# Optimization experiments

Measured on AMD Instinct MI355X. Metric: run time of the kernel, lower is better.

Reference implementation:

```python
import math
import jax, jax.numpy as jnp
from jax import lax
import numpy as np

B, S, D = 64, 257, 768
H, HD = 12, 64  # heads, head_dim; D == H*HD


def setup_inputs() -> dict:
    key = jax.random.key(0)
    ks = jax.random.split(key, 12)
    sc = 0.02
    return {
        "hidden_states": jax.random.normal(ks[0], (B, S, D), jnp.float32),
        "Wq": jax.random.normal(ks[1], (D, D), jnp.float32) * sc,
        "bq": jax.random.normal(ks[2], (D,), jnp.float32) * sc,
        "Wk": jax.random.normal(ks[3], (D, D), jnp.float32) * sc,
        "bk": jax.random.normal(ks[4], (D,), jnp.float32) * sc,
        "Wv": jax.random.normal(ks[5], (D, D), jnp.float32) * sc,
        "bv": jax.random.normal(ks[6], (D,), jnp.float32) * sc,
        "Wo": jax.random.normal(ks[7], (D, D), jnp.float32) * sc,
        "bo": jax.random.normal(ks[8], (D,), jnp.float32) * sc,
        "conv1_w": jax.random.normal(ks[9], (D, 1, 1, 1), jnp.float32) * sc,
        "conv2_w": jax.random.normal(ks[10], (D, 1, 3, 3), jnp.float32) * sc,
        "conv3_w": jax.random.normal(ks[11], (D, 1, 5, 5), jnp.float32) * sc,
    }


def reference(hidden_states, Wq, bq, Wk, bk, Wv, bv, Wo, bo, conv1_w, conv2_w, conv3_w):
    scale = 1.0 / math.sqrt(HD)
    # Q over full sequence (cls + 256 patches)
    q = (hidden_states @ Wq.T + bq).reshape(B, S, H, HD).transpose(0, 2, 1, 3)  # [B,H,S,HD]
    cls_tok = hidden_states[:, :1]                                   # [B,1,D]
    x = hidden_states[:, 1:].transpose(0, 2, 1).reshape(B, D, 16, 16)  # NCHW
    ctx = jnp.zeros((B, H, S, HD), hidden_states.dtype)
    for cw in (conv1_w, conv2_w, conv3_w):  # depthwise convs, VALID padding
        xb = lax.conv_general_dilated(x, cw, (1, 1), 'VALID',
                                      feature_group_count=D)         # [B,D,h,w]
        xb = xb.reshape(B, D, -1).transpose(0, 2, 1)                  # [B,L-1,D]
        xb = jnp.concatenate([cls_tok, xb], axis=1)                   # [B,L,D]
        L = xb.shape[1]
        k = (xb @ Wk.T + bk).reshape(B, L, H, HD).transpose(0, 2, 1, 3)
        v = (xb @ Wv.T + bv).reshape(B, L, H, HD).transpose(0, 2, 1, 3)
        scores = jnp.einsum('bhqd,bhkd->bhqk', q, k) * scale
        probs = jax.nn.softmax(scores, axis=-1)
        ctx = ctx + jnp.einsum('bhqk,bhkd->bhqd', probs, v)
    ctx = (ctx / 3.0).transpose(0, 2, 1, 3).reshape(B, S, D)
    return ctx @ Wo.T + bo
```

## Files before the change

### kernel.cpp

```cpp
#include <hip/hip_runtime.h>

using bf16   = __bf16;
using bf16x4 = __bf16 __attribute__((ext_vector_type(4)));
using bf16x8 = __bf16 __attribute__((ext_vector_type(8)));
using f32x4  = float __attribute__((ext_vector_type(4)));

#define MFMA_BF16(a, b, c) __builtin_amdgcn_mfma_f32_16x16x32_bf16((a), (b), (c), 0, 0, 0)

constexpr int BATCH = 64, SEQ = 257, DIM = 768, NH = 12;
constexpr size_t WE = (size_t)DIM * DIM;

__device__ inline void gload_lds16(const bf16* g, bf16* l) {
  __builtin_amdgcn_global_load_lds(
      (const __attribute__((address_space(1))) void*)g,
      (__attribute__((address_space(3))) void*)l, 16, 0, 0);
}

__global__ __launch_bounds__(256) void cvt_weights(
    const float* __restrict__ wq, const float* __restrict__ wk,
    const float* __restrict__ wv, const float* __restrict__ wo,
    bf16* __restrict__ dst) {
  const size_t i = (size_t)blockIdx.x * 256 + threadIdx.x;
  const size_t per = WE / 4;
  if (i >= 4 * per) return;
  const float* srcs[4] = {wq, wk, wv, wo};
  const float4 f = ((const float4*)srcs[i / per])[i % per];
  bf16* o = dst + i * 4;
  o[0] = (bf16)f.x; o[1] = (bf16)f.y; o[2] = (bf16)f.z; o[3] = (bf16)f.w;
}

__global__ __launch_bounds__(256) void cvt_hs(const float* __restrict__ src,
                                              bf16* __restrict__ dst, int n4) {
  const int i = blockIdx.x * 256 + threadIdx.x;
  if (i >= n4) return;
  const float4 f = ((const float4*)src)[i];
  bf16* o = dst + (size_t)i * 4;
  o[0] = (bf16)f.x; o[1] = (bf16)f.y; o[2] = (bf16)f.z; o[3] = (bf16)f.w;
}

template <int KS>
__global__ __launch_bounds__(256) void conv_kernel(
    const float* __restrict__ hs, const float* __restrict__ cw, bf16* __restrict__ xb) {
  constexpr int OW = 17 - KS;
  constexpr int NOUT = OW * OW;
  constexpr int L = NOUT + 1;
  constexpr int KSQ = KS * KS;
  constexpr int NP = (NOUT + 7) / 8;
  __shared__ float hsl[256][36];
  __shared__ float wsm[32][KSQ];

  const int t = threadIdx.x;
  const int b = blockIdx.y;
  const int c0 = blockIdx.x * 32;

  const float* src = hs + ((size_t)b * SEQ + 1 + t) * DIM + c0;
#pragma unroll
  for (int j = 0; j < 8; ++j) *(float4*)&hsl[t][4 * j] = ((const float4*)src)[j];

  if (t < 32) {
#pragma unroll
    for (int q = 0; q < KSQ; ++q) wsm[t][q] = cw[(size_t)(c0 + t) * KSQ + q];
    const float cv = hs[(size_t)b * SEQ * DIM + c0 + t];
    xb[(size_t)b * L * DIM + c0 + t] = (bf16)cv;
  }
  __syncthreads();

  const int c = t & 31, pg = t >> 5;
#pragma unroll
  for (int i = 0; i < NP; ++i) {
    const int p = pg * NP + i;
    if (p < NOUT) {
      const int oi = p / OW, oj = p - oi * OW;
      float a = 0.f;
#pragma unroll
      for (int di = 0; di < KS; ++di)
#pragma unroll
        for (int dj = 0; dj < KS; ++dj)
          a += hsl[(oi + di) * 16 + oj + dj][c] * wsm[c][di * KS + dj];
      xb[((size_t)b * L + 1 + p) * DIM + c0 + c] = (bf16)a;
    }
  }
}

template <int OUT>
__global__ __launch_bounds__(256, 4) void gemm_lds_kernel(
    const bf16* __restrict__ A, const bf16* __restrict__ W,
    const float* __restrict__ bias0, const float* __restrict__ bias1,
    void* __restrict__ Y0, void* __restrict__ Y1, int M, int L, int Lv, int nN) {
  constexpr int BUF_E = 128 * 32;
  __shared__ alignas(16) bf16 sm[6 * BUF_E];
  bf16* smA = sm;
  bf16* smB = sm + 3 * BUF_E;

  const int tid = threadIdx.x;
  const int lane = tid & 63;
  const int w = tid >> 6;

  const int nwg = gridDim.x;
  const int orig = blockIdx.x;
  const int nq = nwg >> 3, rr = nwg & 7, xcd = orig & 7, base = orig >> 3;
  const int wgid = (xcd < rr ? xcd * (nq + 1) : rr * (nq + 1) + (xcd - rr) * nq) + base;
  const int tM = wgid / nN, tN = wgid - tM * nN;

  const int wr = (w >> 1) * 64, wc = (w & 1) * 64;
  const int rl = lane & 15;
  const int g = lane >> 4;
  const int kqs = ((g ^ ((rl >> 1) & 3)) << 3);

  const int sr = lane >> 2;
  const int sk = (((lane & 3) ^ ((sr >> 1) & 3)) << 3);
  const int r0 = w * 32 + sr;
  const int r1 = w * 32 + 16 + sr;
  long ga0 = (long)tM * 128 + r0; if (ga0 >= M) ga0 = M - 1;
  long ga1 = (long)tM * 128 + r1; if (ga1 >= M) ga1 = M - 1;
  const bf16* pa0 = A + ga0 * DIM + sk;
  const bf16* pa1 = A + ga1 * DIM + sk;
  const bf16* pb0 = W + ((size_t)tN * 128 + r0) * DIM + sk;
  const bf16* pb1 = W + ((size_t)tN * 128 + r1) * DIM + sk;
  const int lbase = (w * 32) * 32;

  const f32x4 zero4 = {0.f, 0.f, 0.f, 0.f};
  f32x4 acc[4][4];
#pragma unroll
  for (int m = 0; m < 4; ++m)
#pragma unroll
    for (int n = 0; n < 4; ++n) acc[m][n] = zero4;

  constexpr int NT = DIM / 32;

#define STAGE(kt_, buf_)                                      \
  do {                                                        \
    const int kb_ = (kt_) * 32;                               \
    bf16* a_ = smA + (buf_) * BUF_E + lbase;                  \
    bf16* b_ = smB + (buf_) * BUF_E + lbase;                  \
    gload_lds16(pa0 + kb_, a_);                               \
    gload_lds16(pa1 + kb_, a_ + 512);                         \
    gload_lds16(pb0 + kb_, b_);                               \
    gload_lds16(pb1 + kb_, b_ + 512);                         \
  } while (0)

  STAGE(0, 0);
  STAGE(1, 1);
  asm volatile("s_waitcnt vmcnt(4)" ::: "memory");
  __builtin_amdgcn_s_barrier();
  __builtin_amdgcn_sched_barrier(0);

  int buf = 0;
  for (int kt = 0; kt < NT; ++kt) {
    const bf16* Ac = smA + buf * BUF_E;
    const bf16* Bc = smB + buf * BUF_E;
    bf16x8 af[4], bfr[4];
#pragma unroll
    for (int m = 0; m < 4; ++m) af[m] = *(const bf16x8*)&Ac[(wr + m * 16 + rl) * 32 + kqs];
#pragma unroll
    for (int n = 0; n < 4; ++n) bfr[n] = *(const bf16x8*)&Bc[(wc + n * 16 + rl) * 32 + kqs];
#pragma unroll
    for (int m = 0; m < 4; ++m)
#pragma unroll
      for (int n = 0; n < 4; ++n) acc[m][n] = MFMA_BF16(af[m], bfr[n], acc[m][n]);

    if (kt + 2 < NT) {
      const int nb = buf + 2 >= 3 ? buf - 1 : buf + 2;
      STAGE(kt + 2, nb);
    }
    if (kt + 1 < NT) {
      if (kt + 2 < NT) asm volatile("s_waitcnt vmcnt(4)" ::: "memory");
      else             asm volatile("s_waitcnt vmcnt(0)" ::: "memory");
      __builtin_amdgcn_s_barrier();
      __builtin_amdgcn_sched_barrier(0);
    }
    buf = buf == 2 ? 0 : buf + 1;
  }
#undef STAGE

  if constexpr (OUT == 3) {
#pragma unroll
    for (int n = 0; n < 4; ++n) {
      const int gcol = tN * 128 + wc + n * 16 + rl;
      const float bia = bias0[gcol];
#pragma unroll
      for (int m = 0; m < 4; ++m) {
#pragma unroll
        for (int i = 0; i < 4; ++i) {
          const long grow = (long)tM * 128 + wr + m * 16 + g * 4 + i;
          if (grow < M) ((float*)Y0)[grow * DIM + gcol] = acc[m][n][i] + bia;
        }
      }
    }
    return;
  }

  constexpr int TP = 136;
  bf16* smT = sm;
  __syncthreads();

  const bool vpath = (OUT == 1) && (tN >= 6);
  if (vpath) {
#pragma unroll
    for (int n = 0; n < 4; ++n) {
      const int col = wc + n * 16 + rl;
      const float bia = bias1[tN * 128 + col - 768];
#pragma unroll
      for (int m = 0; m < 4; ++m) {
        const int row = wr + m * 16 + g * 4;
        bf16x4 v4;
#pragma unroll
        for (int i = 0; i < 4; ++i) v4[i] = (bf16)(acc[m][n][i] + bia);
        *(bf16x4*)(smT + col * TP + row) = v4;
      }
    }
    __syncthreads();
    bf16* vout = (bf16*)Y1;
    const int tNv = tN - 6;
#pragma unroll
    for (int it = 0; it < 8; ++it) {
      const int c = it * 256 + tid;
      const int coll = c >> 4;
      const int rw0 = (c & 15) * 8;
      const long g2 = (long)tM * 128 + rw0;
      if (g2 < M) {
        const int b2 = (int)(g2 / L);
        const int l2 = (int)(g2 - (long)b2 * L);
        const int cv = tNv * 128 + coll;
        bf16* dst = vout + (((size_t)b2 * NH + (cv >> 6)) * 64 + (cv & 63)) * Lv;
        const bf16x8 v = *(const bf16x8*)(smT + coll * TP + rw0);
        if (l2 + 8 <= L) {
          *(bf16x8*)(dst + l2) = v;
        } else {
#pragma unroll
          for (int j = 0; j < 8; ++j) {
            const long g3 = g2 + j;
            const int b3 = (int)(g3 / L), l3 = (int)(g3 - (long)b3 * L);
            vout[(((size_t)b3 * NH + (cv >> 6)) * 64 + (cv & 63)) * Lv + l3] = v[j];
          }
        }
      }
    }
  } else {
    const float scale = (OUT == 0) ? 0.125f : 1.f;
#pragma unroll
    for (int n = 0; n < 4; ++n) {
      const int col = wc + n * 16 + rl;
      const float bia = bias0[tN * 128 + col];
#pragma unroll
      for (int m = 0; m < 4; ++m) {
#pragma unroll
        for (int i = 0; i < 4; ++i) {
          const int row = wr + m * 16 + g * 4 + i;
          smT[row * TP + col] = (bf16)((acc[m][n][i] + bia) * scale);
        }
      }
    }
    __syncthreads();
    bf16* kout = (bf16*)Y0;
#pragma unroll
    for (int it = 0; it < 8; ++it) {
      const int c = it * 256 + tid;
      const int row = c >> 4;
      const int col0 = (c & 15) * 8;
      const long g2 = (long)tM * 128 + row;
      if (g2 < M) {
        const int b2 = (int)(g2 / L);
        const int l2 = (int)(g2 - (long)b2 * L);
        const int gc = tN * 128 + col0;
        const bf16x8 v = *(const bf16x8*)(smT + row * TP + col0);
        int dchunk = (gc & 63) >> 3;
        if constexpr (OUT == 1) dchunk ^= (l2 & 7);
        *(bf16x8*)(kout + (((size_t)b2 * NH + (gc >> 6)) * L + l2) * 64 + dchunk * 8) = v;
      }
    }
  }
}

template <int L, int BRANCH>
__global__ __launch_bounds__(256, 2) void attn_kernel(
    const bf16* __restrict__ qb, const bf16* __restrict__ kb, const bf16* __restrict__ vb,
    float* __restrict__ ctx, bf16* __restrict__ xbuf, int Lv) {
  constexpr int LK16 = (L + 15) & ~15;
  constexpr int NKT = LK16 / 16;
  constexpr int LP32 = (L + 31) & ~31;
  constexpr int NK32 = LP32 / 32;
  constexpr int PSTR = LP32 + 8;
  __shared__ alignas(16) bf16 Ks[LK16 * 64];
  __shared__ alignas(16) bf16 Ps[64 * PSTR];

  const int tid = threadIdx.x, lane = tid & 63, w = tid >> 6;
  const int orig = blockIdx.x;
  const int nper = gridDim.x >> 3;
  const int bh = (orig & 7) * nper + (orig >> 3);
  const int b = bh / NH, h = bh % NH;
  const int cl = lane & 15, g = lane >> 4;

  const bf16* kbase = kb + (size_t)bh * L * 64;
  for (int c = tid; c < LK16 * 8; c += 256)
    gload_lds16(kbase + (size_t)c * 8, Ks + (size_t)c * 8);
  __syncthreads();

  const bf16* vbase = vb + (size_t)bh * 64 * Lv;

  for (int qt = 0; qt < 5; ++qt) {
    int sq = qt * 64 + w * 16 + cl;
    if (sq > 256) sq = 256;
    const bf16* qrow = qb + ((size_t)bh * 257 + sq) * 64 + g * 8;
    const bf16x8 aq0 = *(const bf16x8*)qrow;
    const bf16x8 aq1 = *(const bf16x8*)(qrow + 32);

    float sums[4] = {0.f, 0.f, 0.f, 0.f};
    const int prow0 = (w * 16 + g * 4) * PSTR + cl;
#pragma unroll
    for (int kt = 0; kt < NKT; ++kt) {
      const int key0 = kt * 16 + cl;
      const int sw = key0 & 7;
      const char* krow = (const char*)Ks + key0 * 128;
      const bf16x8 bk0 = *(const bf16x8*)(krow + ((g ^ sw) << 4));
      const bf16x8 bk1 = *(const bf16x8*)(krow + (((4 + g) ^ sw) << 4));
      f32x4 z = {0.f, 0.f, 0.f, 0.f};
      z = MFMA_BF16(aq0, bk0, z);
      z = MFMA_BF16(aq1, bk1, z);
      const bool valid = key0 < L;
#pragma unroll
      for (int j = 0; j < 4; ++j) {
        const float p = valid ? __expf(z[j]) : 0.f;
        sums[j] += p;
        Ps[prow0 + j * PSTR + kt * 16] = (bf16)p;
      }
    }
    if constexpr (LP32 > LK16) {
#pragma unroll
      for (int j = 0; j < 4; ++j) Ps[prow0 + j * PSTR + LK16] = (bf16)0.f;
    }

    bf16x8 vr0[4], vr1[4];
#pragma unroll
    for (int nt = 0; nt < 4; ++nt)
      vr0[nt] = *(const bf16x8*)(vbase + (size_t)(nt * 16 + cl) * Lv + g * 8);

#pragma unroll
    for (int j = 0; j < 4; ++j) {
      sums[j] += __shfl_xor(sums[j], 1);
      sums[j] += __shfl_xor(sums[j], 2);
      sums[j] += __shfl_xor(sums[j], 4);
      sums[j] += __shfl_xor(sums[j], 8);
    }
    float inv[4];
#pragma unroll
    for (int j = 0; j < 4; ++j) inv[j] = 1.f / sums[j];

    f32x4 cacc[4];
#pragma unroll
    for (int nt = 0; nt < 4; ++nt) cacc[nt] = f32x4{0.f, 0.f, 0.f, 0.f};
#pragma unroll
    for (int kt = 0; kt < NK32; ++kt) {
      const bool even = (kt & 1) == 0;
      if (kt + 1 < NK32) {
        int kk = (kt + 1) * 32 + g * 8;
        if (kk > Lv - 8) kk = Lv - 8;
#pragma unroll
        for (int nt = 0; nt < 4; ++nt) {
          const bf16x8 v = *(const bf16x8*)(vbase + (size_t)(nt * 16 + cl) * Lv + kk);
          if (even) vr1[nt] = v; else vr0[nt] = v;
        }
      }
      const bf16x8 ap = *(const bf16x8*)&Ps[(w * 16 + cl) * PSTR + kt * 32 + g * 8];
#pragma unroll
      for (int nt = 0; nt < 4; ++nt)
        cacc[nt] = MFMA_BF16(ap, even ? vr0[nt] : vr1[nt], cacc[nt]);
    }

#pragma unroll
    for (int nt = 0; nt < 4; ++nt) {
#pragma unroll
      for (int i = 0; i < 4; ++i) {
        const int s_q = qt * 64 + w * 16 + g * 4 + i;
        if (s_q < 257) {
          const size_t idx = ((size_t)b * 257 + s_q) * DIM + h * 64 + nt * 16 + cl;
          const float val = cacc[nt][i] * inv[i];
          if constexpr (BRANCH == 0)
            ctx[idx] = val;
          else if constexpr (BRANCH == 1)
            ctx[idx] += val;
          else
            xbuf[idx] = (bf16)((ctx[idx] + val) * (1.f / 3.f));
        }
      }
    }
  }
}

extern "C" void kernel_launch(void* const* d_in, const int* in_sizes, int n_in,
                              void* d_out, int out_size, void* d_ws, size_t ws_size,
                              hipStream_t stream) {
  (void)in_sizes; (void)n_in; (void)out_size; (void)ws_size;
  const float* hs = (const float*)d_in[0];
  const float* Wq = (const float*)d_in[1];
  const float* bq = (const float*)d_in[2];
  const float* Wk = (const float*)d_in[3];
  const float* bk = (const float*)d_in[4];
  const float* Wv = (const float*)d_in[5];
  const float* bv = (const float*)d_in[6];
  const float* Wo = (const float*)d_in[7];
  const float* bo = (const float*)d_in[8];
  const float* c1 = (const float*)d_in[9];
  const float* c2 = (const float*)d_in[10];
  const float* c3 = (const float*)d_in[11];
  float* out = (float*)d_out;

  constexpr size_t QB = (size_t)BATCH * NH * SEQ * 64;
  constexpr size_t XB = (size_t)BATCH * SEQ * DIM;
  constexpr size_t K1 = (size_t)BATCH * NH * 257 * 64;

  bf16* wbf = (bf16*)d_ws;
  bf16* qb = wbf + 4 * WE;
  bf16* xb = qb + QB;
  bf16* kbf = xb + XB;
  bf16* vbf = kbf + K1;
  bf16* hsb = xb;

  cvt_weights<<<dim3((unsigned)((4 * WE / 4 + 255) / 256)), 256, 0, stream>>>(Wq, Wk, Wv, Wo, wbf);
  cvt_hs<<<dim3((BATCH * SEQ * DIM / 4 + 255) / 256), 256, 0, stream>>>(hs, hsb, BATCH * SEQ * DIM / 4);

  gemm_lds_kernel<0><<<dim3(129 * 6), 256, 0, stream>>>(hsb, wbf, bq, bq, qb, qb, BATCH * SEQ, 257, 1, 6);

  conv_kernel<1><<<dim3(24, 64), 256, 0, stream>>>(hs, c1, xb);
  gemm_lds_kernel<1><<<dim3(129 * 12), 256, 0, stream>>>(xb, wbf + WE, bk, bv, kbf, vbf, BATCH * 257, 257, 264, 12);
  attn_kernel<257, 0><<<dim3(768), 256, 0, stream>>>(qb, kbf, vbf, out, xb, 264);

  conv_kernel<3><<<dim3(24, 64), 256, 0, stream>>>(hs, c2, xb);
  gemm_lds_kernel<1><<<dim3(99 * 12), 256, 0, stream>>>(xb, wbf + WE, bk, bv, kbf, vbf, BATCH * 197, 197, 200, 12);
  attn_kernel<197, 1><<<dim3(768), 256, 0, stream>>>(qb, kbf, vbf, out, xb, 200);

  conv_kernel<5><<<dim3(24, 64), 256, 0, stream>>>(hs, c3, xb);
  gemm_lds_kernel<1><<<dim3(73 * 12), 256, 0, stream>>>(xb, wbf + WE, bk, bv, kbf, vbf, BATCH * 145, 145, 152, 12);
  attn_kernel<145, 2><<<dim3(768), 256, 0, stream>>>(qb, kbf, vbf, out, xb, 152);

  gemm_lds_kernel<3><<<dim3(129 * 6), 256, 0, stream>>>(xb, wbf + 3 * WE, bo, bo, out, out, BATCH * SEQ, 257, 1, 6);
}
```

Before: 527.5 us.

## Fold 1x1 conv into K/V weights and fuse QKV and branch KV GEMMs

Pre-scales the Wk and Wv columns by the 1x1 depthwise conv weights, so branch 0's K/V can be computed directly from the hidden states. This lets the Q, K0 and V0 projections run in a single GEMM launch. A small fixup kernel recomputes the CLS-row K/V with the unscaled weights. The 3x3 and 5x5 branch K/V GEMMs are merged into one launch with separate buffers, and the conv1 kernel is dropped, removing launches and improving grid fill. The cost is extra workspace for the duplicated weights and buffers, plus the extra CLS fixup pass.

```diff
diff --git a/kernel.cpp b/kernel.cpp
--- a/kernel.cpp
+++ b/kernel.cpp
@@ -16,17 +16,26 @@
       (__attribute__((address_space(3))) void*)l, 16, 0, 0);
 }
 
-__global__ __launch_bounds__(256) void cvt_weights(
+__global__ __launch_bounds__(256) void cvt_weights6(
     const float* __restrict__ wq, const float* __restrict__ wk,
     const float* __restrict__ wv, const float* __restrict__ wo,
-    bf16* __restrict__ dst) {
+    const float* __restrict__ c1, bf16* __restrict__ dst) {
   const size_t i = (size_t)blockIdx.x * 256 + threadIdx.x;
   const size_t per = WE / 4;
-  if (i >= 4 * per) return;
-  const float* srcs[4] = {wq, wk, wv, wo};
-  const float4 f = ((const float4*)srcs[i / per])[i % per];
+  if (i >= 6 * per) return;
+  const int region = (int)(i / per);
+  const size_t within = i % per;
+  const float* srcs[6] = {wq, wk, wv, wk, wv, wo};
+  const float4 f = ((const float4*)srcs[region])[within];
+  float v[4] = {f.x, f.y, f.z, f.w};
+  if (region == 1 || region == 2) {
+    const int c0 = (int)((within * 4) % DIM);
+#pragma unroll
+    for (int j = 0; j < 4; ++j) v[j] *= c1[c0 + j];
+  }
   bf16* o = dst + i * 4;
-  o[0] = (bf16)f.x; o[1] = (bf16)f.y; o[2] = (bf16)f.z; o[3] = (bf16)f.w;
+#pragma unroll
+  for (int j = 0; j < 4; ++j) o[j] = (bf16)v[j];
 }
 
 __global__ __launch_bounds__(256) void cvt_hs(const float* __restrict__ src,
@@ -83,25 +92,16 @@
 }
 
 template <int OUT>
-__global__ __launch_bounds__(256, 4) void gemm_lds_kernel(
-    const bf16* __restrict__ A, const bf16* __restrict__ W,
-    const float* __restrict__ bias0, const float* __restrict__ bias1,
-    void* __restrict__ Y0, void* __restrict__ Y1, int M, int L, int Lv, int nN) {
+__device__ __forceinline__ void gemm_core(
+    bf16* sm, const bf16* A, const bf16* W,
+    const float* b0, const float* b1, const float* b2,
+    void* Y0, void* Y1, void* Y2, int M, int L, int Lv, int tM, int tN, int tid) {
   constexpr int BUF_E = 128 * 32;
-  __shared__ alignas(16) bf16 sm[6 * BUF_E];
   bf16* smA = sm;
   bf16* smB = sm + 3 * BUF_E;
 
-  const int tid = threadIdx.x;
   const int lane = tid & 63;
   const int w = tid >> 6;
-
-  const int nwg = gridDim.x;
-  const int orig = blockIdx.x;
-  const int nq = nwg >> 3, rr = nwg & 7, xcd = orig & 7, base = orig >> 3;
-  const int wgid = (xcd < rr ? xcd * (nq + 1) : rr * (nq + 1) + (xcd - rr) * nq) + base;
-  const int tM = wgid / nN, tN = wgid - tM * nN;
-
   const int wr = (w >> 1) * 64, wc = (w & 1) * 64;
   const int rl = lane & 15;
   const int g = lane >> 4;
@@ -177,7 +177,7 @@
 #pragma unroll
     for (int n = 0; n < 4; ++n) {
       const int gcol = tN * 128 + wc + n * 16 + rl;
-      const float bia = bias0[gcol];
+      const float bia = b0[gcol];
 #pragma unroll
       for (int m = 0; m < 4; ++m) {
 #pragma unroll
@@ -194,12 +194,16 @@
   bf16* smT = sm;
   __syncthreads();
 
-  const bool vpath = (OUT == 1) && (tN >= 6);
+  const bool vpath = (OUT == 1 && tN >= 6) || (OUT == 4 && tN >= 12);
+  const bool qpath = (OUT == 4 && tN < 6);
+
   if (vpath) {
+    const int cbase = (OUT == 4) ? 1536 : 768;
+    const float* bv_ = (OUT == 4) ? b2 : b1;
 #pragma unroll
     for (int n = 0; n < 4; ++n) {
       const int col = wc + n * 16 + rl;
-      const float bia = bias1[tN * 128 + col - 768];
+      const float bia = bv_[tN * 128 + col - cbase];
 #pragma unroll
       for (int m = 0; m < 4; ++m) {
         const int row = wr + m * 16 + g * 4;
@@ -210,8 +214,8 @@
       }
     }
     __syncthreads();
-    bf16* vout = (bf16*)Y1;
-    const int tNv = tN - 6;
+    bf16* vout = (bf16*)((OUT == 4) ? Y2 : Y1);
+    const int tNv = tN - ((OUT == 4) ? 12 : 6);
 #pragma unroll
     for (int it = 0; it < 8; ++it) {
       const int c = it * 256 + tid;
@@ -219,10 +223,10 @@
       const int rw0 = (c & 15) * 8;
       const long g2 = (long)tM * 128 + rw0;
       if (g2 < M) {
-        const int b2 = (int)(g2 / L);
-        const int l2 = (int)(g2 - (long)b2 * L);
+        const int b2i = (int)(g2 / L);
+        const int l2 = (int)(g2 - (long)b2i * L);
         const int cv = tNv * 128 + coll;
-        bf16* dst = vout + (((size_t)b2 * NH + (cv >> 6)) * 64 + (cv & 63)) * Lv;
+        bf16* dst = vout + (((size_t)b2i * NH + (cv >> 6)) * 64 + (cv & 63)) * Lv;
         const bf16x8 v = *(const bf16x8*)(smT + coll * TP + rw0);
         if (l2 + 8 <= L) {
           *(bf16x8*)(dst + l2) = v;
@@ -237,11 +241,14 @@
       }
     }
   } else {
-    const float scale = (OUT == 0) ? 0.125f : 1.f;
+    const float scale = qpath ? 0.125f : 1.f;
 #pragma unroll
     for (int n = 0; n < 4; ++n) {
       const int col = wc + n * 16 + rl;
-      const float bia = bias0[tN * 128 + col];
+      const int gcol = tN * 128 + col;
+      float bia;
+      if constexpr (OUT == 4) bia = (gcol < 768) ? b0[gcol] : b1[gcol - 768];
+      else                    bia = b0[gcol];
 #pragma unroll
       for (int m = 0; m < 4; ++m) {
 #pragma unroll
@@ -252,7 +259,9 @@
       }
     }
     __syncthreads();
-    bf16* kout = (bf16*)Y0;
+    bf16* kout = (bf16*)((OUT == 4 && !qpath) ? Y1 : Y0);
+    const int coff = (OUT == 4 && !qpath) ? 768 : 0;
+    const bool kswz = !qpath;
 #pragma unroll
     for (int it = 0; it < 8; ++it) {
       const int c = it * 256 + tid;
@@ -260,14 +269,88 @@
       const int col0 = (c & 15) * 8;
       const long g2 = (long)tM * 128 + row;
       if (g2 < M) {
-        const int b2 = (int)(g2 / L);
-        const int l2 = (int)(g2 - (long)b2 * L);
-        const int gc = tN * 128 + col0;
+        const int b2i = (int)(g2 / L);
+        const int l2 = (int)(g2 - (long)b2i * L);
+        const int gc = tN * 128 + col0 - coff;
         const bf16x8 v = *(const bf16x8*)(smT + row * TP + col0);
         int dchunk = (gc & 63) >> 3;
-        if constexpr (OUT == 1) dchunk ^= (l2 & 7);
-        *(bf16x8*)(kout + (((size_t)b2 * NH + (gc >> 6)) * L + l2) * 64 + dchunk * 8) = v;
-      }
+        if (kswz) dchunk ^= (l2 & 7);
+        *(bf16x8*)(kout + (((size_t)b2i * NH + (gc >> 6)) * L + l2) * 64 + dchunk * 8) = v;
+      }
+    }
+  }
+}
+
+__device__ __forceinline__ int m204_swz(int orig, int nwg) {
+  const int nq = nwg >> 3, rr = nwg & 7, xcd = orig & 7, base = orig >> 3;
+  return (xcd < rr ? xcd * (nq + 1) : rr * (nq + 1) + (xcd - rr) * nq) + base;
+}
+
+__global__ __launch_bounds__(256, 4) void gemm_qkv0_kernel(
+    const bf16* __restrict__ A, const bf16* __restrict__ W,
+    const float* __restrict__ bq, const float* __restrict__ bk, const float* __restrict__ bv,
+    bf16* __restrict__ qb, bf16* __restrict__ kb, bf16* __restrict__ vb) {
+  constexpr int BUF_E = 128 * 32;
+  __shared__ alignas(16) bf16 sm[6 * BUF_E];
+  const int wgid = m204_swz(blockIdx.x, gridDim.x);
+  const int tM = wgid / 18, tN = wgid - tM * 18;
+  gemm_core<4>(sm, A, W, bq, bk, bv, qb, kb, vb, BATCH * SEQ, 257, 264, tM, tN, threadIdx.x);
+}
+
+__global__ __launch_bounds__(256, 4) void gemm_kv12_kernel(
+    const bf16* __restrict__ A1, const bf16* __restrict__ A2, const bf16* __restrict__ W,
+    const float* __restrict__ bk, const float* __restrict__ bv,
+    bf16* __restrict__ k1, bf16* __restrict__ v1,
+    bf16* __restrict__ k2, bf16* __restrict__ v2) {
+  constexpr int BUF_E = 128 * 32;
+  __shared__ alignas(16) bf16 sm[6 * BUF_E];
+  const int wgid = m204_swz(blockIdx.x, gridDim.x);
+  if (wgid < 1188) {
+    const int tM = wgid / 12, tN = wgid - tM * 12;
+    gemm_core<1>(sm, A1, W, bk, bv, nullptr, k1, v1, nullptr, BATCH * 197, 197, 200, tM, tN, threadIdx.x);
+  } else {
+    const int l = wgid - 1188;
+    const int tM = l / 12, tN = l - tM * 12;
+    gemm_core<1>(sm, A2, W, bk, bv, nullptr, k2, v2, nullptr, BATCH * 145, 145, 152, tM, tN, threadIdx.x);
+  }
+}
+
+__global__ __launch_bounds__(256, 4) void gemm_o_kernel(
+    const bf16* __restrict__ A, const bf16* __restrict__ W,
+    const float* __restrict__ bo, float* __restrict__ out) {
+  constexpr int BUF_E = 128 * 32;
+  __shared__ alignas(16) bf16 sm[6 * BUF_E];
+  const int wgid = m204_swz(blockIdx.x, gridDim.x);
+  const int tM = wgid / 6, tN = wgid - tM * 6;
+  gemm_core<3>(sm, A, W, bo, nullptr, nullptr, out, nullptr, nullptr, BATCH * SEQ, 257, 1, tM, tN, threadIdx.x);
+}
+
+__global__ __launch_bounds__(256) void cls_fixup_kernel(
+    const bf16* __restrict__ hsb, const bf16* __restrict__ wk, const bf16* __restrict__ wv,
+    const float* __restrict__ bk, const float* __restrict__ bv,
+    bf16* __restrict__ k12, bf16* __restrict__ v12) {
+  __shared__ float hrow[DIM];
+  const int b = blockIdx.y, tile = blockIdx.x, t = threadIdx.x;
+  for (int i = t; i < DIM; i += 256) hrow[i] = (float)hsb[(size_t)b * SEQ * DIM + i];
+  __syncthreads();
+  const bool isv = tile >= 6;
+  const int o = (tile - (isv ? 6 : 0)) * 128 + (t >> 1);
+  const int half = t & 1;
+  const bf16* wrow = (isv ? wv : wk) + (size_t)o * DIM + half * 384;
+  float s = 0.f;
+#pragma unroll 4
+  for (int k = 0; k < 48; ++k) {
+    const bf16x8 wv8 = *(const bf16x8*)(wrow + k * 8);
+#pragma unroll
+    for (int j = 0; j < 8; ++j) s += hrow[half * 384 + k * 8 + j] * (float)wv8[j];
+  }
+  s += __shfl_xor(s, 1);
+  if (!half) {
+    s += (isv ? bv : bk)[o];
+    if (!isv) {
+      k12[(((size_t)b * NH + (o >> 6)) * 257) * 64 + (o & 63)] = (bf16)s;
+    } else {
+      v12[(((size_t)b * NH + (o >> 6)) * 64 + (o & 63)) * 264] = (bf16)s;
     }
   }
 }
@@ -407,31 +490,34 @@
 
   constexpr size_t QB = (size_t)BATCH * NH * SEQ * 64;
   constexpr size_t XB = (size_t)BATCH * SEQ * DIM;
-  constexpr size_t K1 = (size_t)BATCH * NH * 257 * 64;
+  constexpr size_t K12 = (size_t)BATCH * NH * 257 * 64;
+  constexpr size_t V12 = (size_t)BATCH * NH * 64 * 264;
+  constexpr size_t XB3 = (size_t)BATCH * 145 * DIM;
+  constexpr size_t K3 = (size_t)BATCH * NH * 145 * 64;
 
   bf16* wbf = (bf16*)d_ws;
-  bf16* qb = wbf + 4 * WE;
-  bf16* xb = qb + QB;
-  bf16* kbf = xb + XB;
-  bf16* vbf = kbf + K1;
+  bf16* qb  = wbf + 6 * WE;
+  bf16* xb  = qb + QB;
+  bf16* k12 = xb + XB;
+  bf16* v12 = k12 + K12;
+  bf16* xb3 = v12 + V12;
+  bf16* k3  = xb3 + XB3;
+  bf16* v3  = k3 + K3;
   bf16* hsb = xb;
 
-  cvt_weights<<<dim3((unsigned)((4 * WE / 4 + 255) / 256)), 256, 0, stream>>>(Wq, Wk, Wv, Wo, wbf);
+  cvt_weights6<<<dim3((unsigned)((6 * WE / 4 + 255) / 256)), 256, 0, stream>>>(Wq, Wk, Wv, Wo, c1, wbf);
   cvt_hs<<<dim3((BATCH * SEQ * DIM / 4 + 255) / 256), 256, 0, stream>>>(hs, hsb, BATCH * SEQ * DIM / 4);
 
-  gemm_lds_kernel<0><<<dim3(129 * 6), 256, 0, stream>>>(hsb, wbf, bq, bq, qb, qb, BATCH * SEQ, 257, 1, 6);
-
-  conv_kernel<1><<<dim3(24, 64), 256, 0, stream>>>(hs, c1, xb);
-  gemm_lds_kernel<1><<<dim3(129 * 12), 256, 0, stream>>>(xb, wbf + WE, bk, bv, kbf, vbf, BATCH * 257, 257, 264, 12);
-  attn_kernel<257, 0><<<dim3(768), 256, 0, stream>>>(qb, kbf, vbf, out, xb, 264);
+  gemm_qkv0_kernel<<<dim3(129 * 18), 256, 0, stream>>>(hsb, wbf, bq, bk, bv, qb, k12, v12);
+  cls_fixup_kernel<<<dim3(12, 64), 256, 0, stream>>>(hsb, wbf + 3 * WE, wbf + 4 * WE, bk, bv, k12, v12);
+  attn_kernel<257, 0><<<dim3(768), 256, 0, stream>>>(qb, k12, v12, out, xb, 264);
 
   conv_kernel<3><<<dim3(24, 64), 256, 0, stream>>>(hs, c2, xb);
-  gemm_lds_kernel<1><<<dim3(99 * 12), 256, 0, stream>>>(xb, wbf + WE, bk, bv, kbf, vbf, BATCH * 197, 197, 200, 12);
-  attn_kernel<197, 1><<<dim3(768), 256, 0, stream>>>(qb, kbf, vbf, out, xb, 200);
-
-  conv_kernel<5><<<dim3(24, 64), 256, 0, stream>>>(hs, c3, xb);
-  gemm_lds_kernel<1><<<dim3(73 * 12), 256, 0, stream>>>(xb, wbf + WE, bk, bv, kbf, vbf, BATCH * 145, 145, 152, 12);
-  attn_kernel<145, 2><<<dim3(768), 256, 0, stream>>>(qb, kbf, vbf, out, xb, 152);
-
-  gemm_lds_kernel<3><<<dim3(129 * 6), 256, 0, stream>>>(xb, wbf + 3 * WE, bo, bo, out, out, BATCH * SEQ, 257, 1, 6);
-}
+  conv_kernel<5><<<dim3(24, 64), 256, 0, stream>>>(hs, c3, xb3);
+  gemm_kv12_kernel<<<dim3(1188 + 876), 256, 0, stream>>>(xb, xb3, wbf + 3 * WE, bk, bv,
+                                                         k12, v12, k3, v3);
+  attn_kernel<197, 1><<<dim3(768), 256, 0, stream>>>(qb, k12, v12, out, xb, 200);
+  attn_kernel<145, 2><<<dim3(768), 256, 0, stream>>>(qb, k3, v3, out, xb, 152);
+
+  gemm_o_kernel<<<dim3(129 * 6), 256, 0, stream>>>(xb, wbf + 5 * WE, bo, out);
+}
```

New measurement: 514.6 us. -2.4%, faster.
